# Kernel tuning notes

Measured on AMD Instinct MI355X. Metric: run time of the kernel, lower is better.

Reference implementation:

```python
import jax, jax.numpy as jnp
import numpy as np

E = 1024   # emb_dim
H = 1024   # hidden_size
L = 2      # num_layers
V = 50257  # vocab_size
S = 2048   # encoder input length
T = 2048   # decoder target length


def setup_inputs() -> dict:
    key = jax.random.key(0)
    ks = jax.random.split(key, 16)
    s = 0.02  # init scale
    f32 = jnp.float32
    return {
        "inputs": jax.random.randint(ks[0], (1, S), 0, V),
        "outputs": jax.random.randint(ks[1], (1, T), 0, V),
        "sos": 1,
        "enc_emb": jax.random.normal(ks[2], (V, E), f32) * s,
        "dec_emb": jax.random.normal(ks[3], (V, E), f32) * s,
        # Stacked LSTM weights; layer-0 input dim == E == H so layers stack.
        "enc_Wih": jax.random.normal(ks[4], (L, 4 * H, H), f32) * s,
        "enc_Whh": jax.random.normal(ks[5], (L, 4 * H, H), f32) * s,
        "enc_bih": jax.random.normal(ks[6], (L, 4 * H), f32) * s,
        "enc_bhh": jax.random.normal(ks[7], (L, 4 * H), f32) * s,
        "dec_Wih": jax.random.normal(ks[8], (L, 4 * H, H), f32) * s,
        "dec_Whh": jax.random.normal(ks[9], (L, 4 * H, H), f32) * s,
        "dec_bih": jax.random.normal(ks[10], (L, 4 * H), f32) * s,
        "dec_bhh": jax.random.normal(ks[11], (L, 4 * H), f32) * s,
        "lin_W": jax.random.normal(ks[12], (V, H), f32) * s,
        "lin_b": jax.random.normal(ks[13], (V,), f32) * s,
    }


def _run_stack(xs, Wih, Whh, bih, bhh, h0, c0):
    # xs: [S, E]; Wih/Whh: [L, 4H, H]; h0/c0: [L, H]
    # PyTorch LSTM gate order: i, f, g, o.
    h_fin, c_fin = [], []
    for l in range(Wih.shape[0]):
        Wi, Wh, bi, bh = Wih[l], Whh[l], bih[l], bhh[l]

        def step(carry, x, Wi=Wi, Wh=Wh, bi=bi, bh=bh):
            h, c = carry
            g = Wi @ x + bi + Wh @ h + bh           # [4H]
            i, f, gg, o = jnp.split(g, 4)
            c = jax.nn.sigmoid(f) * c + jax.nn.sigmoid(i) * jnp.tanh(gg)
            h = jax.nn.sigmoid(o) * jnp.tanh(c)
            return (h, c), h

        (h, c), xs = jax.lax.scan(step, (h0[l], c0[l]), xs)
        h_fin.append(h)
        c_fin.append(c)
    return xs, jnp.stack(h_fin), jnp.stack(c_fin)


def reference(inputs, outputs, sos, enc_emb, dec_emb,
              enc_Wih, enc_Whh, enc_bih, enc_bhh,
              dec_Wih, dec_Whh, dec_bih, dec_bhh,
              lin_W, lin_b):
    # Encoder over the source sequence (batch == 1, squeezed away).
    x = enc_emb[inputs[0]]                       # [S, E]
    z = jnp.zeros((L, H), dtype=x.dtype)
    _, hN, cN = _run_stack(x, enc_Wih, enc_Whh, enc_bih, enc_bhh, z, z)
    # Full teacher forcing: decoder inputs are [sos, outputs[:, :-1]].
    dec_tokens = jnp.concatenate(
        [jnp.array([sos], dtype=outputs.dtype), outputs[0, :-1]])
    y = dec_emb[dec_tokens]                      # [T, E]
    dec_out, _, _ = _run_stack(y, dec_Wih, dec_Whh, dec_bih, dec_bhh, hN, cN)
    logits = dec_out @ lin_W.T + lin_b           # [T, V]
    return logits
```

## Files before the change

kernel.cpp:

```cpp
#include <hip/hip_runtime.h>
#include <hip/hip_bf16.h>
#include <math.h>

#define S_LEN 2048
#define T_LEN 2048
#define HID   1024
#define GATES 4096
#define VOCAB 50257

typedef unsigned int u32;
typedef unsigned short u16;
typedef unsigned long long ull;
typedef u32 u32x4 __attribute__((ext_vector_type(4)));
typedef float f32x4 __attribute__((ext_vector_type(4)));
typedef short s16x8 __attribute__((ext_vector_type(8)));

__device__ __forceinline__ float fsig_(float x)  { return 1.0f / (1.0f + __expf(-x)); }
__device__ __forceinline__ float ftanh_(float x) { float e = __expf(2.0f * x); return 1.0f - 2.0f / (e + 1.0f); }

__device__ __forceinline__ u32 bf16rne(float x) {
  u32 u = __float_as_uint(x);
  return (u + 0x7FFFu + ((u >> 16) & 1u)) >> 16;
}
__device__ __forceinline__ float bf16tof(u32 b) { return __uint_as_float(b << 16); }

__device__ __forceinline__ void pollpipe2(const ull* p0, const ull* p1, u32 want,
                                          ull& ra, ull& rb) {
  ull r0a, r0b, r1a, r1b, stmp;
  u32 par;
  const ull wantv = ((ull)want) << 32;
  asm volatile(
    "s_waitcnt vmcnt(0)\n\t"
    "global_load_dwordx2 %[r0a], %[p0], off sc0 sc1\n\t"
    "global_load_dwordx2 %[r0b], %[p1], off sc0 sc1\n\t"
    "1:\n\t"
    "global_load_dwordx2 %[r1a], %[p0], off sc0 sc1\n\t"
    "global_load_dwordx2 %[r1b], %[p1], off sc0 sc1\n\t"
    "s_waitcnt vmcnt(2)\n\t"
    "v_cmp_lt_u64 vcc, %[r0a], %[wv]\n\t"
    "s_mov_b64 %[st], vcc\n\t"
    "v_cmp_lt_u64 vcc, %[r0b], %[wv]\n\t"
    "s_or_b64 vcc, vcc, %[st]\n\t"
    "s_cbranch_vccz 2f\n\t"
    "global_load_dwordx2 %[r0a], %[p0], off sc0 sc1\n\t"
    "global_load_dwordx2 %[r0b], %[p1], off sc0 sc1\n\t"
    "s_waitcnt vmcnt(2)\n\t"
    "v_cmp_lt_u64 vcc, %[r1a], %[wv]\n\t"
    "s_mov_b64 %[st], vcc\n\t"
    "v_cmp_lt_u64 vcc, %[r1b], %[wv]\n\t"
    "s_or_b64 vcc, vcc, %[st]\n\t"
    "s_cbranch_vccz 3f\n\t"
    "s_branch 1b\n\t"
    "2:\n\t"
    "s_mov_b32 %[par], 0\n\t"
    "s_branch 4f\n\t"
    "3:\n\t"
    "s_mov_b32 %[par], 1\n\t"
    "4:\n\t"
    "s_waitcnt vmcnt(0)"
    : [r0a]"=&v"(r0a), [r0b]"=&v"(r0b), [r1a]"=&v"(r1a), [r1b]"=&v"(r1b),
      [st]"=&s"(stmp), [par]"=&s"(par)
    : [p0]"v"(p0), [p1]"v"(p1), [wv]"v"(wantv)
    : "vcc", "memory");
  ra = par ? r1a : r0a;
  rb = par ? r1b : r0b;
}

__global__ void zero_f4(float4* __restrict__ p, size_t n4) {
  size_t i = (size_t)blockIdx.x * blockDim.x + threadIdx.x;
  size_t stride = (size_t)gridDim.x * blockDim.x;
  for (; i < n4; i += stride) p[i] = make_float4(0.f, 0.f, 0.f, 0.f);
}

__global__ void build_dec_tokens(const int* __restrict__ outputs, const int* __restrict__ sos,
                                 int* __restrict__ toks, int T) {
  int t = blockIdx.x * blockDim.x + threadIdx.x;
  if (t < T) toks[t] = (t == 0) ? sos[0] : outputs[t - 1];
}

__global__ void xsplit(const float* __restrict__ x, u16* __restrict__ hi,
                       u16* __restrict__ lo, int n) {
  int i = blockIdx.x * 256 + threadIdx.x;
  if (i < n) {
    float v = x[i];
    u32 h = bf16rne(v);
    hi[i] = (u16)h;
    lo[i] = (u16)bf16rne(v - bf16tof(h));
  }
}

__global__ __launch_bounds__(256) void gemm_logits(
    const u16* __restrict__ Xhi, const u16* __restrict__ Xlo,
    const float* __restrict__ W, const float* __restrict__ b,
    float* __restrict__ C, int M, int N, int K)
{
  __shared__ u16 Bhi[64][40];
  __shared__ u16 Blo[64][40];
  const int tid = threadIdx.x;
  const int wv  = tid >> 6;
  const int l   = tid & 63;
  const int l15 = l & 15;
  const int kro = (l >> 4) * 8;
  const int m0  = blockIdx.y * 128;
  const int n0  = blockIdx.x * 64;
  const int srow = tid >> 2;
  const int skp  = (tid & 3) * 8;

  f32x4 acc[2][4] = {};

  for (int k0 = 0; k0 < K; k0 += 32) {
    float w[8] = {0.f};
    {
      int wr = n0 + srow;
      if (wr < N) {
        const float4 a = *(const float4*)(W + (size_t)wr * K + k0 + skp);
        const float4 c = *(const float4*)(W + (size_t)wr * K + k0 + skp + 4);
        w[0] = a.x; w[1] = a.y; w[2] = a.z; w[3] = a.w;
        w[4] = c.x; w[5] = c.y; w[6] = c.z; w[7] = c.w;
      }
    }
    __syncthreads();
#pragma unroll
    for (int e = 0; e < 8; ++e) {
      u32 h = bf16rne(w[e]);
      Bhi[srow][skp + e] = (u16)h;
      Blo[srow][skp + e] = (u16)bf16rne(w[e] - bf16tof(h));
    }
    __syncthreads();

    const size_t xoff0 = (size_t)(m0 + wv * 32 + l15) * K + k0 + kro;
    const size_t xoff1 = xoff0 + (size_t)16 * K;
    s16x8 ah0 = *(const s16x8*)(Xhi + xoff0);
    s16x8 al0 = *(const s16x8*)(Xlo + xoff0);
    s16x8 ah1 = *(const s16x8*)(Xhi + xoff1);
    s16x8 al1 = *(const s16x8*)(Xlo + xoff1);
#pragma unroll
    for (int tn = 0; tn < 4; ++tn) {
      s16x8 bh = *(const s16x8*)&Bhi[tn * 16 + l15][kro];
      s16x8 bl = *(const s16x8*)&Blo[tn * 16 + l15][kro];
      acc[0][tn] = __builtin_amdgcn_mfma_f32_16x16x32_bf16(ah0, bh, acc[0][tn], 0, 0, 0);
      acc[0][tn] = __builtin_amdgcn_mfma_f32_16x16x32_bf16(al0, bh, acc[0][tn], 0, 0, 0);
      acc[0][tn] = __builtin_amdgcn_mfma_f32_16x16x32_bf16(ah0, bl, acc[0][tn], 0, 0, 0);
      acc[1][tn] = __builtin_amdgcn_mfma_f32_16x16x32_bf16(ah1, bh, acc[1][tn], 0, 0, 0);
      acc[1][tn] = __builtin_amdgcn_mfma_f32_16x16x32_bf16(al1, bh, acc[1][tn], 0, 0, 0);
      acc[1][tn] = __builtin_amdgcn_mfma_f32_16x16x32_bf16(ah1, bl, acc[1][tn], 0, 0, 0);
    }
  }

#pragma unroll
  for (int tm = 0; tm < 2; ++tm)
#pragma unroll
    for (int tn = 0; tn < 4; ++tn) {
      int n = n0 + tn * 16 + l15;
      if (n < N) {
        float bias = b[n];
#pragma unroll
        for (int r = 0; r < 4; ++r) {
          int m = m0 + wv * 32 + tm * 16 + (l >> 4) * 4 + r;
          C[(size_t)m * N + n] = acc[tm][tn][r] + bias;
        }
      }
    }
}

__global__ __launch_bounds__(512, 1) void lstm2(
    const float* __restrict__ emb,  const int* __restrict__ toks,
    const float* __restrict__ Wi0,  const float* __restrict__ Wh0,
    const float* __restrict__ bi0,  const float* __restrict__ bh0,
    const float* __restrict__ Wi1,  const float* __restrict__ Wh1,
    const float* __restrict__ bi1,  const float* __restrict__ bh1,
    const float* __restrict__ h00,  const float* __restrict__ c00,
    const float* __restrict__ h01,  const float* __restrict__ c01,
    ull* __restrict__ s0, ull* __restrict__ s1,
    float* __restrict__ hf0, float* __restrict__ cf0,
    float* __restrict__ hf1, float* __restrict__ cf1,
    float* __restrict__ dec_out, int T)
{
  const int tid = threadIdx.x;
  const int wg  = blockIdx.x;
  const bool isL0 = (wg < 128);
  const int wgl = isL0 ? wg : wg - 128;

  const int lane16 = tid & 15;
  const int rloc = tid >> 4;
  const int jloc = rloc & 7;
  const int gate = rloc >> 3;
  const int grow = gate * HID + wgl * 8 + jloc;

  __shared__ float lds_x[2][HID];
  __shared__ float lds_h[HID];
  __shared__ float lds_g[32];
  __shared__ float lds_c[8];

  const float* Wi = isL0 ? Wi0 : Wi1;
  const float* Wh = isL0 ? Wh0 : Wh1;
  const float breg = (isL0 ? (bi0[grow] + bh0[grow]) : (bi1[grow] + bh1[grow]));

  f32x4 Wir[16], Whr[16];
  {
    const f32x4* wi = (const f32x4*)(Wi + (size_t)grow * HID);
    const f32x4* wh = (const f32x4*)(Wh + (size_t)grow * HID);
#pragma unroll
    for (int i = 0; i < 16; ++i) {
      Wir[i] = wi[lane16 + i * 16];
      Whr[i] = wh[lane16 + i * 16];
    }
  }

  {
    const float* hini = isL0 ? h00 : h01;
    const float* cini = isL0 ? c00 : c01;
    if (tid < 8) lds_c[tid] = cini[wgl * 8 + tid];
    if (tid < 256) ((float4*)lds_h)[tid] = ((const float4*)hini)[tid];
    if (isL0 && tid < 256) {
      int tok = toks[0];
      ((float4*)lds_x[0])[tid] = ((const float4*)(emb + (size_t)tok * HID))[tid];
    }
  }
  __syncthreads();

  ull* s_mine = isL0 ? s0 : s1;

  for (int t = 0; t < T; ++t) {
    const int cur = t & 1;

    if (isL0) {
      if (t > 0) {
        ull va, vb;
        pollpipe2(s0 + (size_t)(t - 1) * HID + 2 * tid,
                  s0 + (size_t)(t - 1) * HID + 2 * tid + 1, (u32)t, va, vb);
        lds_h[2 * tid]     = __uint_as_float((u32)va);
        lds_h[2 * tid + 1] = __uint_as_float((u32)vb);
      }
    } else {
      {
        ull va, vb;
        pollpipe2(s0 + (size_t)t * HID + 2 * tid,
                  s0 + (size_t)t * HID + 2 * tid + 1, (u32)(t + 1), va, vb);
        lds_x[0][2 * tid]     = __uint_as_float((u32)va);
        lds_x[0][2 * tid + 1] = __uint_as_float((u32)vb);
      }
      if (t > 0) {
        ull va, vb;
        pollpipe2(s1 + (size_t)(t - 1) * HID + 2 * tid,
                  s1 + (size_t)(t - 1) * HID + 2 * tid + 1, (u32)t, va, vb);
        lds_h[2 * tid]     = __uint_as_float((u32)va);
        lds_h[2 * tid + 1] = __uint_as_float((u32)vb);
      }
    }
    __syncthreads();

    if (isL0 && tid < 256 && t + 1 < T) {
      int tok = toks[t + 1];
      ((float4*)lds_x[cur ^ 1])[tid] = ((const float4*)(emb + (size_t)tok * HID))[tid];
    }

    const float* xbuf = isL0 ? lds_x[cur] : lds_x[0];
    float p0 = 0.f, p1 = 0.f, p2 = 0.f, p3 = 0.f;
#pragma unroll
    for (int i = 0; i < 16; ++i) {
      const float4 xv = *(const float4*)&xbuf[(lane16 << 2) + (i << 6)];
      p0 = fmaf(Wir[i].x, xv.x, p0);
      p1 = fmaf(Wir[i].y, xv.y, p1);
      p2 = fmaf(Wir[i].z, xv.z, p2);
      p3 = fmaf(Wir[i].w, xv.w, p3);
    }
#pragma unroll
    for (int i = 0; i < 16; ++i) {
      const float4 hv = *(const float4*)&lds_h[(lane16 << 2) + (i << 6)];
      p0 = fmaf(Whr[i].x, hv.x, p0);
      p1 = fmaf(Whr[i].y, hv.y, p1);
      p2 = fmaf(Whr[i].z, hv.z, p2);
      p3 = fmaf(Whr[i].w, hv.w, p3);
    }
    float sum = (p0 + p1) + (p2 + p3);
    sum += __shfl_xor(sum, 1);
    sum += __shfl_xor(sum, 2);
    sum += __shfl_xor(sum, 4);
    sum += __shfl_xor(sum, 8);
    if (lane16 == 0) lds_g[rloc] = sum + breg;
    __syncthreads();

    if (tid < 8) {
      const float gi = lds_g[tid];
      const float gf = lds_g[8 + tid];
      const float gg = lds_g[16 + tid];
      const float go = lds_g[24 + tid];
      const float c = fsig_(gf) * lds_c[tid] + fsig_(gi) * ftanh_(gg);
      const float h = fsig_(go) * ftanh_(c);
      lds_c[tid] = c;
      const int col = wgl * 8 + tid;
      const ull pk = ((ull)(u32)(t + 1) << 32) | (ull)__float_as_uint(h);
      __hip_atomic_store(&s_mine[(size_t)t * HID + col], pk,
                         __ATOMIC_RELAXED, __HIP_MEMORY_SCOPE_AGENT);
      if (!isL0 && dec_out) dec_out[(size_t)t * HID + col] = h;
      if (t == T - 1) {
        if (isL0) { if (hf0) hf0[col] = h; if (cf0) cf0[col] = c; }
        else      { if (hf1) hf1[col] = h; if (cf1) cf1[col] = c; }
      }
    }
  }
}

extern "C" void kernel_launch(void* const* d_in, const int* in_sizes, int n_in,
                              void* d_out, int out_size, void* d_ws, size_t ws_size,
                              hipStream_t stream) {
  const int*   inputs  = (const int*)d_in[0];
  const int*   outputs = (const int*)d_in[1];
  const int*   sos     = (const int*)d_in[2];
  const float* enc_emb = (const float*)d_in[3];
  const float* dec_emb = (const float*)d_in[4];
  const float* enc_Wih = (const float*)d_in[5];
  const float* enc_Whh = (const float*)d_in[6];
  const float* enc_bih = (const float*)d_in[7];
  const float* enc_bhh = (const float*)d_in[8];
  const float* dec_Wih = (const float*)d_in[9];
  const float* dec_Whh = (const float*)d_in[10];
  const float* dec_bih = (const float*)d_in[11];
  const float* dec_bhh = (const float*)d_in[12];
  const float* lin_W   = (const float*)d_in[13];
  const float* lin_b   = (const float*)d_in[14];

  float* out = (float*)d_out;
  ull* s0e = (ull*)d_out;
  ull* s1e = s0e + 2097152;
  ull* s0d = s1e + 2097152;
  ull* s1d = s0d + 2097152;

  char* ws = (char*)d_ws;
  float* zerosv = (float*)(ws + 0);
  float* hf0    = (float*)(ws + 4096);
  float* cf0    = (float*)(ws + 8192);
  float* hf1    = (float*)(ws + 12288);
  float* cf1    = (float*)(ws + 16384);
  int*   dtoks  = (int*)(ws + 20480);
  float* B2     = (float*)(ws + ((size_t)1 << 20));
  u16*   Xhi    = (u16*)(ws + ((size_t)10 << 20));
  u16*   Xlo    = (u16*)(ws + ((size_t)15 << 20));

  const size_t WOFF = (size_t)GATES * HID;

  zero_f4<<<2048, 256, 0, stream>>>((float4*)d_out, 4194304);
  zero_f4<<<1, 256, 0, stream>>>((float4*)zerosv, 256);
  build_dec_tokens<<<8, 256, 0, stream>>>(outputs, sos, dtoks, T_LEN);

  lstm2<<<256, 512, 0, stream>>>(
      enc_emb, inputs,
      enc_Wih, enc_Whh, enc_bih, enc_bhh,
      enc_Wih + WOFF, enc_Whh + WOFF, enc_bih + GATES, enc_bhh + GATES,
      zerosv, zerosv, zerosv, zerosv,
      s0e, s1e, hf0, cf0, hf1, cf1, nullptr, S_LEN);

  lstm2<<<256, 512, 0, stream>>>(
      dec_emb, dtoks,
      dec_Wih, dec_Whh, dec_bih, dec_bhh,
      dec_Wih + WOFF, dec_Whh + WOFF, dec_bih + GATES, dec_bhh + GATES,
      hf0, cf0, hf1, cf1,
      s0d, s1d, nullptr, nullptr, nullptr, nullptr, B2, T_LEN);

  xsplit<<<(T_LEN * HID + 255) / 256, 256, 0, stream>>>(B2, Xhi, Xlo, T_LEN * HID);
  dim3 gemmV_grid((VOCAB + 63) / 64, T_LEN / 128);
  gemm_logits<<<gemmV_grid, 256, 0, stream>>>(Xhi, Xlo, lin_W, lin_b, out,
                                              T_LEN, VOCAB, HID);
}
```

Before: 12.87 ms.

## Assign one wavefront per hidden unit and merge layer-1 polls into one loop

The LSTM recurrence kernel is remapped so each 64-lane wavefront owns all four gate rows of one hidden unit and keeps the cell state in a register. The gate nonlinearity then runs inside the wave after a full 64-lane shuffle reduction, which removes the LDS gate buffer and one block barrier per timestep. For layer 1, the two spin-polls (layer-0 output for step t and its own h for step t-1) are merged into a single pollpipe4 loop so the two waits overlap. Weight preloading now uses inline asm dwordx4 loads. The cost is a longer shuffle reduction, plus a trailing barrier at the end of each step.

```diff
diff --git a/kernel.cpp b/kernel.cpp
--- a/kernel.cpp
+++ b/kernel.cpp
@@ -23,6 +23,18 @@
   return (u + 0x7FFFu + ((u >> 16) & 1u)) >> 16;
 }
 __device__ __forceinline__ float bf16tof(u32 b) { return __uint_as_float(b << 16); }
+
+__device__ __forceinline__ void wload4(const float* base, f32x4& w0, f32x4& w1,
+                                       f32x4& w2, f32x4& w3) {
+  asm volatile(
+    "global_load_dwordx4 %0, %4, off\n\t"
+    "global_load_dwordx4 %1, %4, off offset:1024\n\t"
+    "global_load_dwordx4 %2, %4, off offset:2048\n\t"
+    "global_load_dwordx4 %3, %4, off offset:3072\n\t"
+    "s_waitcnt vmcnt(0)"
+    : "=&v"(w0), "=&v"(w1), "=&v"(w2), "=&v"(w3)
+    : "v"(base) : "memory");
+}
 
 __device__ __forceinline__ void pollpipe2(const ull* p0, const ull* p1, u32 want,
                                           ull& ra, ull& rb) {
@@ -66,6 +78,68 @@
   rb = par ? r1b : r0b;
 }
 
+__device__ __forceinline__ void pollpipe4(const ull* p0, const ull* p1, u32 wantA,
+                                          const ull* q0, const ull* q1, u32 wantB,
+                                          ull& ra, ull& rb, ull& rc, ull& rd) {
+  ull r0a, r0b, r0c, r0d, r1a, r1b, r1c, r1d, stmp;
+  u32 par;
+  const ull wA = ((ull)wantA) << 32;
+  const ull wB = ((ull)wantB) << 32;
+  asm volatile(
+    "s_waitcnt vmcnt(0)\n\t"
+    "global_load_dwordx2 %[r0a], %[p0], off sc0 sc1\n\t"
+    "global_load_dwordx2 %[r0b], %[p1], off sc0 sc1\n\t"
+    "global_load_dwordx2 %[r0c], %[q0], off sc0 sc1\n\t"
+    "global_load_dwordx2 %[r0d], %[q1], off sc0 sc1\n\t"
+    "1:\n\t"
+    "global_load_dwordx2 %[r1a], %[p0], off sc0 sc1\n\t"
+    "global_load_dwordx2 %[r1b], %[p1], off sc0 sc1\n\t"
+    "global_load_dwordx2 %[r1c], %[q0], off sc0 sc1\n\t"
+    "global_load_dwordx2 %[r1d], %[q1], off sc0 sc1\n\t"
+    "s_waitcnt vmcnt(4)\n\t"
+    "v_cmp_lt_u64 vcc, %[r0a], %[wA]\n\t"
+    "s_mov_b64 %[st], vcc\n\t"
+    "v_cmp_lt_u64 vcc, %[r0b], %[wA]\n\t"
+    "s_or_b64 %[st], vcc, %[st]\n\t"
+    "v_cmp_lt_u64 vcc, %[r0c], %[wB]\n\t"
+    "s_or_b64 %[st], vcc, %[st]\n\t"
+    "v_cmp_lt_u64 vcc, %[r0d], %[wB]\n\t"
+    "s_or_b64 vcc, vcc, %[st]\n\t"
+    "s_cbranch_vccz 2f\n\t"
+    "global_load_dwordx2 %[r0a], %[p0], off sc0 sc1\n\t"
+    "global_load_dwordx2 %[r0b], %[p1], off sc0 sc1\n\t"
+    "global_load_dwordx2 %[r0c], %[q0], off sc0 sc1\n\t"
+    "global_load_dwordx2 %[r0d], %[q1], off sc0 sc1\n\t"
+    "s_waitcnt vmcnt(4)\n\t"
+    "v_cmp_lt_u64 vcc, %[r1a], %[wA]\n\t"
+    "s_mov_b64 %[st], vcc\n\t"
+    "v_cmp_lt_u64 vcc, %[r1b], %[wA]\n\t"
+    "s_or_b64 %[st], vcc, %[st]\n\t"
+    "v_cmp_lt_u64 vcc, %[r1c], %[wB]\n\t"
+    "s_or_b64 %[st], vcc, %[st]\n\t"
+    "v_cmp_lt_u64 vcc, %[r1d], %[wB]\n\t"
+    "s_or_b64 vcc, vcc, %[st]\n\t"
+    "s_cbranch_vccz 3f\n\t"
+    "s_branch 1b\n\t"
+    "2:\n\t"
+    "s_mov_b32 %[par], 0\n\t"
+    "s_branch 4f\n\t"
+    "3:\n\t"
+    "s_mov_b32 %[par], 1\n\t"
+    "4:\n\t"
+    "s_waitcnt vmcnt(0)"
+    : [r0a]"=&v"(r0a), [r0b]"=&v"(r0b), [r0c]"=&v"(r0c), [r0d]"=&v"(r0d),
+      [r1a]"=&v"(r1a), [r1b]"=&v"(r1b), [r1c]"=&v"(r1c), [r1d]"=&v"(r1d),
+      [st]"=&s"(stmp), [par]"=&s"(par)
+    : [p0]"v"(p0), [p1]"v"(p1), [q0]"v"(q0), [q1]"v"(q1),
+      [wA]"v"(wA), [wB]"v"(wB)
+    : "vcc", "memory");
+  ra = par ? r1a : r0a;
+  rb = par ? r1b : r0b;
+  rc = par ? r1c : r0c;
+  rd = par ? r1d : r0d;
+}
+
 __global__ void zero_f4(float4* __restrict__ p, size_t n4) {
   size_t i = (size_t)blockIdx.x * blockDim.x + threadIdx.x;
   size_t stride = (size_t)gridDim.x * blockDim.x;
@@ -176,41 +250,34 @@
     float* __restrict__ hf1, float* __restrict__ cf1,
     float* __restrict__ dec_out, int T)
 {
-  const int tid = threadIdx.x;
-  const int wg  = blockIdx.x;
+  const int tid   = threadIdx.x;
+  const int wg    = blockIdx.x;
   const bool isL0 = (wg < 128);
-  const int wgl = isL0 ? wg : wg - 128;
-
-  const int lane16 = tid & 15;
-  const int rloc = tid >> 4;
-  const int jloc = rloc & 7;
-  const int gate = rloc >> 3;
-  const int grow = gate * HID + wgl * 8 + jloc;
+  const int wgl   = isL0 ? wg : wg - 128;
+  const int wlane = tid & 63;
+  const int unit  = tid >> 6;
 
   __shared__ float lds_x[2][HID];
   __shared__ float lds_h[HID];
-  __shared__ float lds_g[32];
-  __shared__ float lds_c[8];
 
   const float* Wi = isL0 ? Wi0 : Wi1;
   const float* Wh = isL0 ? Wh0 : Wh1;
-  const float breg = (isL0 ? (bi0[grow] + bh0[grow]) : (bi1[grow] + bh1[grow]));
-
-  f32x4 Wir[16], Whr[16];
-  {
-    const f32x4* wi = (const f32x4*)(Wi + (size_t)grow * HID);
-    const f32x4* wh = (const f32x4*)(Wh + (size_t)grow * HID);
-#pragma unroll
-    for (int i = 0; i < 16; ++i) {
-      Wir[i] = wi[lane16 + i * 16];
-      Whr[i] = wh[lane16 + i * 16];
-    }
+  const float* bi = isL0 ? bi0 : bi1;
+  const float* bh = isL0 ? bh0 : bh1;
+
+  float bias[4];
+  f32x4 Wt[4][8];
+#pragma unroll
+  for (int r = 0; r < 4; ++r) {
+    const int growr = r * HID + wgl * 8 + unit;
+    bias[r] = bi[growr] + bh[growr];
+    wload4(Wi + (size_t)growr * HID + 4 * wlane, Wt[r][0], Wt[r][1], Wt[r][2], Wt[r][3]);
+    wload4(Wh + (size_t)growr * HID + 4 * wlane, Wt[r][4], Wt[r][5], Wt[r][6], Wt[r][7]);
   }
 
+  float creg = (isL0 ? c00 : c01)[wgl * 8 + unit];
   {
     const float* hini = isL0 ? h00 : h01;
-    const float* cini = isL0 ? c00 : c01;
-    if (tid < 8) lds_c[tid] = cini[wgl * 8 + tid];
     if (tid < 256) ((float4*)lds_h)[tid] = ((const float4*)hini)[tid];
     if (isL0 && tid < 256) {
       int tok = toks[0];
@@ -233,19 +300,22 @@
         lds_h[2 * tid + 1] = __uint_as_float((u32)vb);
       }
     } else {
-      {
+      if (t == 0) {
         ull va, vb;
-        pollpipe2(s0 + (size_t)t * HID + 2 * tid,
-                  s0 + (size_t)t * HID + 2 * tid + 1, (u32)(t + 1), va, vb);
+        pollpipe2(s0 + 2 * tid, s0 + 2 * tid + 1, 1u, va, vb);
         lds_x[0][2 * tid]     = __uint_as_float((u32)va);
         lds_x[0][2 * tid + 1] = __uint_as_float((u32)vb);
-      }
-      if (t > 0) {
-        ull va, vb;
-        pollpipe2(s1 + (size_t)(t - 1) * HID + 2 * tid,
-                  s1 + (size_t)(t - 1) * HID + 2 * tid + 1, (u32)t, va, vb);
-        lds_h[2 * tid]     = __uint_as_float((u32)va);
-        lds_h[2 * tid + 1] = __uint_as_float((u32)vb);
+      } else {
+        ull va, vb, vc, vd;
+        pollpipe4(s0 + (size_t)t * HID + 2 * tid,
+                  s0 + (size_t)t * HID + 2 * tid + 1, (u32)(t + 1),
+                  s1 + (size_t)(t - 1) * HID + 2 * tid,
+                  s1 + (size_t)(t - 1) * HID + 2 * tid + 1, (u32)t,
+                  va, vb, vc, vd);
+        lds_x[0][2 * tid]     = __uint_as_float((u32)va);
+        lds_x[0][2 * tid + 1] = __uint_as_float((u32)vb);
+        lds_h[2 * tid]        = __uint_as_float((u32)vc);
+        lds_h[2 * tid + 1]    = __uint_as_float((u32)vd);
       }
     }
     __syncthreads();
@@ -256,49 +326,52 @@
     }
 
     const float* xbuf = isL0 ? lds_x[cur] : lds_x[0];
-    float p0 = 0.f, p1 = 0.f, p2 = 0.f, p3 = 0.f;
-#pragma unroll
-    for (int i = 0; i < 16; ++i) {
-      const float4 xv = *(const float4*)&xbuf[(lane16 << 2) + (i << 6)];
-      p0 = fmaf(Wir[i].x, xv.x, p0);
-      p1 = fmaf(Wir[i].y, xv.y, p1);
-      p2 = fmaf(Wir[i].z, xv.z, p2);
-      p3 = fmaf(Wir[i].w, xv.w, p3);
-    }
-#pragma unroll
-    for (int i = 0; i < 16; ++i) {
-      const float4 hv = *(const float4*)&lds_h[(lane16 << 2) + (i << 6)];
-      p0 = fmaf(Whr[i].x, hv.x, p0);
-      p1 = fmaf(Whr[i].y, hv.y, p1);
-      p2 = fmaf(Whr[i].z, hv.z, p2);
-      p3 = fmaf(Whr[i].w, hv.w, p3);
-    }
-    float sum = (p0 + p1) + (p2 + p3);
-    sum += __shfl_xor(sum, 1);
-    sum += __shfl_xor(sum, 2);
-    sum += __shfl_xor(sum, 4);
-    sum += __shfl_xor(sum, 8);
-    if (lane16 == 0) lds_g[rloc] = sum + breg;
-    __syncthreads();
-
-    if (tid < 8) {
-      const float gi = lds_g[tid];
-      const float gf = lds_g[8 + tid];
-      const float gg = lds_g[16 + tid];
-      const float go = lds_g[24 + tid];
-      const float c = fsig_(gf) * lds_c[tid] + fsig_(gi) * ftanh_(gg);
-      const float h = fsig_(go) * ftanh_(c);
-      lds_c[tid] = c;
-      const int col = wgl * 8 + tid;
+    float4 xh[8];
+#pragma unroll
+    for (int k = 0; k < 4; ++k) xh[k]     = ((const float4*)xbuf)[64 * k + wlane];
+#pragma unroll
+    for (int k = 0; k < 4; ++k) xh[4 + k] = ((const float4*)lds_h)[64 * k + wlane];
+
+    float sr[4];
+#pragma unroll
+    for (int r = 0; r < 4; ++r) {
+      float a0 = 0.f, a1 = 0.f, a2 = 0.f, a3 = 0.f;
+#pragma unroll
+      for (int k = 0; k < 8; ++k) {
+        a0 = fmaf(Wt[r][k].x, xh[k].x, a0);
+        a1 = fmaf(Wt[r][k].y, xh[k].y, a1);
+        a2 = fmaf(Wt[r][k].z, xh[k].z, a2);
+        a3 = fmaf(Wt[r][k].w, xh[k].w, a3);
+      }
+      sr[r] = (a0 + a1) + (a2 + a3);
+    }
+
+#pragma unroll
+    for (int r = 0; r < 4; ++r) {
+      float v = sr[r];
+      v += __shfl_xor(v, 1);
+      v += __shfl_xor(v, 2);
+      v += __shfl_xor(v, 4);
+      v += __shfl_xor(v, 8);
+      v += __shfl_xor(v, 16);
+      v += __shfl_xor(v, 32);
+      sr[r] = v + bias[r];
+    }
+
+    creg = fsig_(sr[1]) * creg + fsig_(sr[0]) * ftanh_(sr[2]);
+    const float h = fsig_(sr[3]) * ftanh_(creg);
+    if (wlane == 0) {
+      const int col = wgl * 8 + unit;
       const ull pk = ((ull)(u32)(t + 1) << 32) | (ull)__float_as_uint(h);
       __hip_atomic_store(&s_mine[(size_t)t * HID + col], pk,
                          __ATOMIC_RELAXED, __HIP_MEMORY_SCOPE_AGENT);
       if (!isL0 && dec_out) dec_out[(size_t)t * HID + col] = h;
       if (t == T - 1) {
-        if (isL0) { if (hf0) hf0[col] = h; if (cf0) cf0[col] = c; }
-        else      { if (hf1) hf1[col] = h; if (cf1) cf1[col] = c; }
-      }
-    }
+        if (isL0) { if (hf0) hf0[col] = h; if (cf0) cf0[col] = creg; }
+        else      { if (hf1) hf1[col] = h; if (cf1) cf1[col] = creg; }
+      }
+    }
+    __syncthreads();
   }
 }
 
```

New measurement: 15.09 ms. 1.17x slower.

## Pack two bf16 hidden values per flag slot and merge layer-1 polls

Applied to the files above, without the earlier changes.

Each LSTM workgroup now publishes two hidden units as bf16 in a single 64-bit flag+payload word, which halves the number of slots each consumer thread polls per timestep. Layer 1 issues its h-load speculatively alongside the x poll and re-polls only if some lane's flag is stale. The handoff of inter-block state gets cheaper, but the recurrent h and the layer-1 input are rounded to bf16, which adds numerical error that accumulates over time.

```diff
diff --git a/kernel.cpp b/kernel.cpp
--- a/kernel.cpp
+++ b/kernel.cpp
@@ -7,11 +7,11 @@
 #define HID   1024
 #define GATES 4096
 #define VOCAB 50257
+#define SLOTS 512
 
 typedef unsigned int u32;
 typedef unsigned short u16;
 typedef unsigned long long ull;
-typedef u32 u32x4 __attribute__((ext_vector_type(4)));
 typedef float f32x4 __attribute__((ext_vector_type(4)));
 typedef short s16x8 __attribute__((ext_vector_type(8)));
 
@@ -24,31 +24,21 @@
 }
 __device__ __forceinline__ float bf16tof(u32 b) { return __uint_as_float(b << 16); }
 
-__device__ __forceinline__ void pollpipe2(const ull* p0, const ull* p1, u32 want,
-                                          ull& ra, ull& rb) {
-  ull r0a, r0b, r1a, r1b, stmp;
+__device__ __forceinline__ ull pollpipe1(const ull* p, u32 want) {
+  ull r0, r1;
   u32 par;
   const ull wantv = ((ull)want) << 32;
   asm volatile(
     "s_waitcnt vmcnt(0)\n\t"
-    "global_load_dwordx2 %[r0a], %[p0], off sc0 sc1\n\t"
-    "global_load_dwordx2 %[r0b], %[p1], off sc0 sc1\n\t"
+    "global_load_dwordx2 %[r0], %[p], off sc0 sc1\n\t"
     "1:\n\t"
-    "global_load_dwordx2 %[r1a], %[p0], off sc0 sc1\n\t"
-    "global_load_dwordx2 %[r1b], %[p1], off sc0 sc1\n\t"
-    "s_waitcnt vmcnt(2)\n\t"
-    "v_cmp_lt_u64 vcc, %[r0a], %[wv]\n\t"
-    "s_mov_b64 %[st], vcc\n\t"
-    "v_cmp_lt_u64 vcc, %[r0b], %[wv]\n\t"
-    "s_or_b64 vcc, vcc, %[st]\n\t"
+    "global_load_dwordx2 %[r1], %[p], off sc0 sc1\n\t"
+    "s_waitcnt vmcnt(1)\n\t"
+    "v_cmp_lt_u64 vcc, %[r0], %[wv]\n\t"
     "s_cbranch_vccz 2f\n\t"
-    "global_load_dwordx2 %[r0a], %[p0], off sc0 sc1\n\t"
-    "global_load_dwordx2 %[r0b], %[p1], off sc0 sc1\n\t"
-    "s_waitcnt vmcnt(2)\n\t"
-    "v_cmp_lt_u64 vcc, %[r1a], %[wv]\n\t"
-    "s_mov_b64 %[st], vcc\n\t"
-    "v_cmp_lt_u64 vcc, %[r1b], %[wv]\n\t"
-    "s_or_b64 vcc, vcc, %[st]\n\t"
+    "global_load_dwordx2 %[r0], %[p], off sc0 sc1\n\t"
+    "s_waitcnt vmcnt(1)\n\t"
+    "v_cmp_lt_u64 vcc, %[r1], %[wv]\n\t"
     "s_cbranch_vccz 3f\n\t"
     "s_branch 1b\n\t"
     "2:\n\t"
@@ -58,12 +48,42 @@
     "s_mov_b32 %[par], 1\n\t"
     "4:\n\t"
     "s_waitcnt vmcnt(0)"
-    : [r0a]"=&v"(r0a), [r0b]"=&v"(r0b), [r1a]"=&v"(r1a), [r1b]"=&v"(r1b),
-      [st]"=&s"(stmp), [par]"=&s"(par)
-    : [p0]"v"(p0), [p1]"v"(p1), [wv]"v"(wantv)
+    : [r0]"=&v"(r0), [r1]"=&v"(r1), [par]"=&s"(par)
+    : [p]"v"(p), [wv]"v"(wantv)
     : "vcc", "memory");
-  ra = par ? r1a : r0a;
-  rb = par ? r1b : r0b;
+  return par ? r1 : r0;
+}
+
+__device__ __forceinline__ ull pollpipe1h(const ull* p, u32 want,
+                                          const ull* q, ull& vh) {
+  ull r0, r1;
+  u32 par;
+  const ull wantv = ((ull)want) << 32;
+  asm volatile(
+    "s_waitcnt vmcnt(0)\n\t"
+    "global_load_dwordx2 %[vh], %[q], off sc0 sc1\n\t"
+    "global_load_dwordx2 %[r0], %[p], off sc0 sc1\n\t"
+    "1:\n\t"
+    "global_load_dwordx2 %[r1], %[p], off sc0 sc1\n\t"
+    "s_waitcnt vmcnt(1)\n\t"
+    "v_cmp_lt_u64 vcc, %[r0], %[wv]\n\t"
+    "s_cbranch_vccz 2f\n\t"
+    "global_load_dwordx2 %[r0], %[p], off sc0 sc1\n\t"
+    "s_waitcnt vmcnt(1)\n\t"
+    "v_cmp_lt_u64 vcc, %[r1], %[wv]\n\t"
+    "s_cbranch_vccz 3f\n\t"
+    "s_branch 1b\n\t"
+    "2:\n\t"
+    "s_mov_b32 %[par], 0\n\t"
+    "s_branch 4f\n\t"
+    "3:\n\t"
+    "s_mov_b32 %[par], 1\n\t"
+    "4:\n\t"
+    "s_waitcnt vmcnt(0)"
+    : [r0]"=&v"(r0), [r1]"=&v"(r1), [par]"=&s"(par), [vh]"=&v"(vh)
+    : [p]"v"(p), [wv]"v"(wantv), [q]"v"(q)
+    : "vcc", "memory");
+  return par ? r1 : r0;
 }
 
 __global__ void zero_f4(float4* __restrict__ p, size_t n4) {
@@ -226,26 +246,25 @@
 
     if (isL0) {
       if (t > 0) {
-        ull va, vb;
-        pollpipe2(s0 + (size_t)(t - 1) * HID + 2 * tid,
-                  s0 + (size_t)(t - 1) * HID + 2 * tid + 1, (u32)t, va, vb);
-        lds_h[2 * tid]     = __uint_as_float((u32)va);
-        lds_h[2 * tid + 1] = __uint_as_float((u32)vb);
+        ull v = pollpipe1(s0 + (size_t)(t - 1) * SLOTS + tid, (u32)t);
+        lds_h[2 * tid]     = bf16tof((u32)v & 0xFFFFu);
+        lds_h[2 * tid + 1] = bf16tof(((u32)v >> 16) & 0xFFFFu);
       }
     } else {
-      {
-        ull va, vb;
-        pollpipe2(s0 + (size_t)t * HID + 2 * tid,
-                  s0 + (size_t)t * HID + 2 * tid + 1, (u32)(t + 1), va, vb);
-        lds_x[0][2 * tid]     = __uint_as_float((u32)va);
-        lds_x[0][2 * tid + 1] = __uint_as_float((u32)vb);
-      }
-      if (t > 0) {
-        ull va, vb;
-        pollpipe2(s1 + (size_t)(t - 1) * HID + 2 * tid,
-                  s1 + (size_t)(t - 1) * HID + 2 * tid + 1, (u32)t, va, vb);
-        lds_h[2 * tid]     = __uint_as_float((u32)va);
-        lds_h[2 * tid + 1] = __uint_as_float((u32)vb);
+      if (t == 0) {
+        ull v = pollpipe1(s0 + tid, 1u);
+        lds_x[0][2 * tid]     = bf16tof((u32)v & 0xFFFFu);
+        lds_x[0][2 * tid + 1] = bf16tof(((u32)v >> 16) & 0xFFFFu);
+      } else {
+        ull vh;
+        ull vx = pollpipe1h(s0 + (size_t)t * SLOTS + tid, (u32)(t + 1),
+                            s1 + (size_t)(t - 1) * SLOTS + tid, vh);
+        if (!__all((u32)(vh >> 32) >= (u32)t))
+          vh = pollpipe1(s1 + (size_t)(t - 1) * SLOTS + tid, (u32)t);
+        lds_x[0][2 * tid]     = bf16tof((u32)vx & 0xFFFFu);
+        lds_x[0][2 * tid + 1] = bf16tof(((u32)vx >> 16) & 0xFFFFu);
+        lds_h[2 * tid]        = bf16tof((u32)vh & 0xFFFFu);
+        lds_h[2 * tid + 1]    = bf16tof(((u32)vh >> 16) & 0xFFFFu);
       }
     }
     __syncthreads();
@@ -281,22 +300,32 @@
     if (lane16 == 0) lds_g[rloc] = sum + breg;
     __syncthreads();
 
-    if (tid < 8) {
-      const float gi = lds_g[tid];
-      const float gf = lds_g[8 + tid];
-      const float gg = lds_g[16 + tid];
-      const float go = lds_g[24 + tid];
-      const float c = fsig_(gf) * lds_c[tid] + fsig_(gi) * ftanh_(gg);
-      const float h = fsig_(go) * ftanh_(c);
-      lds_c[tid] = c;
-      const int col = wgl * 8 + tid;
-      const ull pk = ((ull)(u32)(t + 1) << 32) | (ull)__float_as_uint(h);
-      __hip_atomic_store(&s_mine[(size_t)t * HID + col], pk,
+    if (tid < 4) {
+      const int u0 = 2 * tid;
+      const float c0v = fsig_(lds_g[8 + u0]) * lds_c[u0]
+                      + fsig_(lds_g[u0]) * ftanh_(lds_g[16 + u0]);
+      const float h0v = fsig_(lds_g[24 + u0]) * ftanh_(c0v);
+      const float c1v = fsig_(lds_g[9 + u0]) * lds_c[u0 + 1]
+                      + fsig_(lds_g[1 + u0]) * ftanh_(lds_g[17 + u0]);
+      const float h1v = fsig_(lds_g[25 + u0]) * ftanh_(c1v);
+      lds_c[u0] = c0v; lds_c[u0 + 1] = c1v;
+      const int col = wgl * 8 + u0;
+      const ull pk = ((ull)(u32)(t + 1) << 32)
+                   | (ull)(bf16rne(h0v) | (bf16rne(h1v) << 16));
+      __hip_atomic_store(&s_mine[(size_t)t * SLOTS + wgl * 4 + tid], pk,
                          __ATOMIC_RELAXED, __HIP_MEMORY_SCOPE_AGENT);
-      if (!isL0 && dec_out) dec_out[(size_t)t * HID + col] = h;
+      if (!isL0 && dec_out) {
+        dec_out[(size_t)t * HID + col]     = h0v;
+        dec_out[(size_t)t * HID + col + 1] = h1v;
+      }
       if (t == T - 1) {
-        if (isL0) { if (hf0) hf0[col] = h; if (cf0) cf0[col] = c; }
-        else      { if (hf1) hf1[col] = h; if (cf1) cf1[col] = c; }
+        if (isL0) {
+          if (hf0) { hf0[col] = h0v; hf0[col + 1] = h1v; }
+          if (cf0) { cf0[col] = c0v; cf0[col + 1] = c1v; }
+        } else {
+          if (hf1) { hf1[col] = h0v; hf1[col + 1] = h1v; }
+          if (cf1) { cf1[col] = c0v; cf1[col + 1] = c1v; }
+        }
       }
     }
   }
@@ -323,9 +352,9 @@
 
   float* out = (float*)d_out;
   ull* s0e = (ull*)d_out;
-  ull* s1e = s0e + 2097152;
-  ull* s0d = s1e + 2097152;
-  ull* s1d = s0d + 2097152;
+  ull* s1e = s0e + (size_t)T_LEN * SLOTS;
+  ull* s0d = s1e + (size_t)T_LEN * SLOTS;
+  ull* s1d = s0d + (size_t)T_LEN * SLOTS;
 
   char* ws = (char*)d_ws;
   float* zerosv = (float*)(ws + 0);
@@ -340,7 +369,7 @@
 
   const size_t WOFF = (size_t)GATES * HID;
 
-  zero_f4<<<2048, 256, 0, stream>>>((float4*)d_out, 4194304);
+  zero_f4<<<2048, 256, 0, stream>>>((float4*)d_out, 2097152);
   zero_f4<<<1, 256, 0, stream>>>((float4*)zerosv, 256);
   build_dec_tokens<<<8, 256, 0, stream>>>(outputs, sos, dtoks, T_LEN);
 
```

Result: slower. 13.30 ms (+3.3%).
